# Kernel tuning notes

Hardware: AMD Instinct MI355X
Metric: run time of the kernel (lower is better)

Reference implementation:

```python
import jax, jax.numpy as jnp
import numpy as np

B, T, D, H, FF = 4, 2048, 1024, 16, 4096
HD = D // H
EPS = 1e-5


def layernorm(x, g, b):
    m = jnp.mean(x, axis=-1, keepdims=True)
    v = jnp.var(x, axis=-1, keepdims=True)
    return (x - m) * jax.lax.rsqrt(v + EPS) * g + b


def setup_inputs() -> dict:
    key = jax.random.key(0)
    ks = jax.random.split(key, 12)
    s = lambda fan_in: 1.0 / np.sqrt(fan_in)
    x = jax.random.normal(ks[0], (B, T, D), dtype=jnp.float32)
    mask = jnp.tril(jnp.ones((T, T), dtype=jnp.int32))[None, None]  # [1,1,T,T] causal
    return {
        "x": x,
        "mask": mask,
        "ln1_g": jnp.ones((D,), jnp.float32),
        "ln1_b": jnp.zeros((D,), jnp.float32),
        "ln2_g": jnp.ones((D,), jnp.float32),
        "ln2_b": jnp.zeros((D,), jnp.float32),
        "qkv_w": jax.random.normal(ks[1], (D, 3 * D), jnp.float32) * s(D),
        "out_w": jax.random.normal(ks[2], (D, D), jnp.float32) * s(D),
        "out_b": jnp.zeros((D,), jnp.float32),
        "fc1_w": jax.random.normal(ks[3], (D, FF), jnp.float32) * s(D),
        "fc1_b": jnp.zeros((FF,), jnp.float32),
        "fc2_w": jax.random.normal(ks[4], (FF, D), jnp.float32) * s(FF),
        "fc2_b": jnp.zeros((D,), jnp.float32),
    }


def reference(x, mask, ln1_g, ln1_b, ln2_g, ln2_b, qkv_w, out_w, out_b,
              fc1_w, fc1_b, fc2_w, fc2_b):
    # --- attention sublayer (pre-LN) ---
    h = layernorm(x, ln1_g, ln1_b)
    qkv = h @ qkv_w  # [B,T,3D]
    q, k, v = jnp.split(qkv, 3, axis=-1)
    q = q.reshape(B, T, H, HD).transpose(0, 2, 1, 3)  # [B,H,T,hd]
    k = k.reshape(B, T, H, HD).transpose(0, 2, 1, 3)
    v = v.reshape(B, T, H, HD).transpose(0, 2, 1, 3)
    scale = 1.0 / np.sqrt(HD)
    scores = jnp.einsum('bhqd,bhkd->bhqk', q, k) * scale  # [B,H,T,T]
    scores = jnp.where(mask == 0, -jnp.inf, scores)
    attn = jax.nn.softmax(scores, axis=-1)
    o = jnp.einsum('bhqk,bhkd->bhqd', attn, v)
    o = o.transpose(0, 2, 1, 3).reshape(B, T, D)
    x = x + (o @ out_w + out_b)
    # --- MLP sublayer (pre-LN) ---
    h = layernorm(x, ln2_g, ln2_b)
    h = jax.nn.gelu(h @ fc1_w + fc1_b, approximate=False)
    x = x + (h @ fc2_w + fc2_b)
    return x
```

## Files before the change

### kernel.cpp

```cpp
#include <hip/hip_runtime.h>

typedef unsigned short bfraw;
typedef __attribute__((ext_vector_type(8))) short short8;
typedef __attribute__((ext_vector_type(4))) float f32x4;

__device__ __forceinline__ float b2f(bfraw u){ return __uint_as_float(((unsigned int)u)<<16); }
__device__ __forceinline__ bfraw f2b(float f){
  unsigned int u = __float_as_uint(f);
  return (bfraw)((u + 0x7FFFu + ((u>>16)&1u)) >> 16);
}
__device__ __forceinline__ void store_out(float* p, float v){ *p = v; }
__device__ __forceinline__ void store_out(bfraw* p, float v){ *p = f2b(v); }
__device__ __forceinline__ void gload_lds16(const bfraw* g, short* l) {
  __builtin_amdgcn_global_load_lds((const __attribute__((address_space(1))) void*)g,
                                   (__attribute__((address_space(3))) void*)l, 16, 0, 0);
}

__global__ __launch_bounds__(1024) void transpose_f32_bf16(const float* __restrict__ in,
                                                           bfraw* __restrict__ out,
                                                           int R, int C) {
  __shared__ bfraw tile[64][65];
  const int tx = threadIdx.x, ty = threadIdx.y;
  const int c0 = blockIdx.x*64, r0 = blockIdx.y*64;
  #pragma unroll
  for (int u = 0; u < 4; ++u)
    tile[ty + u*16][tx] = f2b(in[(size_t)(r0 + ty + u*16)*C + c0 + tx]);
  __syncthreads();
  #pragma unroll
  for (int u = 0; u < 4; ++u)
    out[(size_t)(c0 + ty + u*16)*R + r0 + tx] = tile[tx][ty + u*16];
}

__global__ __launch_bounds__(256) void ln_kernel(const float* __restrict__ x,
                                                 const float* __restrict__ g,
                                                 const float* __restrict__ b,
                                                 bfraw* __restrict__ out) {
  const int row = blockIdx.x, tid = threadIdx.x;
  const f32x4 v = ((const f32x4*)(x + (size_t)row*1024))[tid];
  float s  = v[0]+v[1]+v[2]+v[3];
  float s2 = v[0]*v[0]+v[1]*v[1]+v[2]*v[2]+v[3]*v[3];
  #pragma unroll
  for (int off = 1; off < 64; off <<= 1) { s += __shfl_xor(s, off); s2 += __shfl_xor(s2, off); }
  __shared__ float red[8];
  const int wv = tid>>6, ln_ = tid&63;
  if (ln_ == 0) { red[wv] = s; red[4+wv] = s2; }
  __syncthreads();
  float a  = red[0]+red[1]+red[2]+red[3];
  float a2 = red[4]+red[5]+red[6]+red[7];
  float mean = a*(1.0f/1024.0f);
  float var  = a2*(1.0f/1024.0f) - mean*mean;
  float inv  = rsqrtf(var + 1e-5f);
  const f32x4 gr = ((const f32x4*)g)[tid];
  const f32x4 br = ((const f32x4*)b)[tid];
  ushort4 o4;
  o4.x = f2b((v[0]-mean)*inv*gr[0] + br[0]);
  o4.y = f2b((v[1]-mean)*inv*gr[1] + br[1]);
  o4.z = f2b((v[2]-mean)*inv*gr[2] + br[2]);
  o4.w = f2b((v[3]-mean)*inv*gr[3] + br[3]);
  ((ushort4*)(out + (size_t)row*1024))[tid] = o4;
}

template<int EPI, typename OutT>
__global__ __launch_bounds__(256) void gemm_bt(const bfraw* __restrict__ A,
                                               const bfraw* __restrict__ Bt,
                                               const float* __restrict__ bias,
                                               const float* __restrict__ resid,
                                               OutT* __restrict__ C,
                                               int M, int N, int K) {
  __shared__ __align__(16) short As[128*32];
  __shared__ __align__(16) short Bs[128*32];
  const int tid = threadIdx.x;
  const int wave = tid>>6, lane = tid&63;
  const int wm = wave>>1, wn = wave&1;
  const int q = lane>>4, r = lane&15;
  const int bm = blockIdx.x, bn = blockIdx.y;

  const int m0 = tid>>2, c0 = tid&3;
  const bfraw* Ag0 = A  + (size_t)(bm*128      + m0)*K + c0*8;
  const bfraw* Ag1 = A  + (size_t)(bm*128 + 64 + m0)*K + c0*8;
  const bfraw* Bg0 = Bt + (size_t)(bn*128      + m0)*K + c0*8;
  const bfraw* Bg1 = Bt + (size_t)(bn*128 + 64 + m0)*K + c0*8;
  short* Al0 = &As[tid*8];
  short* Al1 = &As[(256+tid)*8];
  short* Bl0 = &Bs[tid*8];
  short* Bl1 = &Bs[(256+tid)*8];

  f32x4 acc[4][4];
  #pragma unroll
  for (int mi = 0; mi < 4; ++mi)
    #pragma unroll
    for (int ni = 0; ni < 4; ++ni)
      acc[mi][ni] = (f32x4){0.f, 0.f, 0.f, 0.f};

  for (int k0 = 0; k0 < K; k0 += 32) {
    __syncthreads();
    gload_lds16(Ag0 + k0, Al0);
    gload_lds16(Ag1 + k0, Al1);
    gload_lds16(Bg0 + k0, Bl0);
    gload_lds16(Bg1 + k0, Bl1);
    __syncthreads();
    short8 af[4], bfr[4];
    #pragma unroll
    for (int mi = 0; mi < 4; ++mi)
      af[mi] = *(const short8*)&As[(wm*64 + mi*16 + r)*32 + q*8];
    #pragma unroll
    for (int ni = 0; ni < 4; ++ni)
      bfr[ni] = *(const short8*)&Bs[(wn*64 + ni*16 + r)*32 + q*8];
    #pragma unroll
    for (int mi = 0; mi < 4; ++mi)
      #pragma unroll
      for (int ni = 0; ni < 4; ++ni)
        acc[mi][ni] = __builtin_amdgcn_mfma_f32_16x16x32_bf16(af[mi], bfr[ni], acc[mi][ni], 0, 0, 0);
  }

  #pragma unroll
  for (int mi = 0; mi < 4; ++mi) {
    #pragma unroll
    for (int ni = 0; ni < 4; ++ni) {
      const int gcol = bn*128 + wn*64 + ni*16 + r;
      float bv = 0.f;
      if constexpr (EPI != 0) bv = bias[gcol];
      #pragma unroll
      for (int rg = 0; rg < 4; ++rg) {
        const int grow = bm*128 + wm*64 + mi*16 + q*4 + rg;
        float val = acc[mi][ni][rg];
        if constexpr (EPI != 0) val += bv;
        if constexpr (EPI == 2) val = 0.5f*val*(1.0f + erff(val*0.70710678118654752f));
        if constexpr (EPI == 1) val += resid[(size_t)grow*N + gcol];
        store_out(&C[(size_t)grow*N + gcol], val);
      }
    }
  }
}

__global__ __launch_bounds__(256) void flash_attn(const bfraw* __restrict__ qkv,
                                                  bfraw* __restrict__ o) {
  __shared__ __align__(16) short Ksh[4096];
  __shared__ __align__(16) short Vts[4096];
  __shared__ __align__(16) short Psh[4096];
  const int tid = threadIdx.x;
  const int w = tid >> 6, lane = tid & 63;
  const int r = lane & 15, qd = lane >> 4;
  const int bb = blockIdx.y >> 4, h = blockIdx.y & 15;
  const size_t hb = (size_t)bb * 2048;
  short* Pw = &Psh[w * 1024];
  const int f0 = tid, f1 = tid + 256;
  const int key0 = f0 >> 3, dc0 = (f0 & 7) * 8;
  const int key1 = f1 >> 3, dc1 = (f1 & 7) * 8;

  for (int pass = 0; pass < 2; ++pass) {
    const int qt = pass ? (31 - (int)blockIdx.x) : (int)blockIdx.x;
    const int q0 = qt * 64;
    const int ntile = qt + 1;

    short8 qf[2];
    {
      const bfraw* qrow = qkv + (hb + q0 + w*16 + r) * 3072 + h*64;
      qf[0] = *(const short8*)(qrow + qd*8);
      qf[1] = *(const short8*)(qrow + qd*8 + 32);
    }

    f32x4 oacc[4];
    #pragma unroll
    for (int nt = 0; nt < 4; ++nt) oacc[nt] = (f32x4){0.f,0.f,0.f,0.f};
    float m_i[4] = {-3.0e38f,-3.0e38f,-3.0e38f,-3.0e38f};
    float l_i[4] = {0.f,0.f,0.f,0.f};

    short8 kpre[2], vpre[2];
    {
      const bfraw* b0 = qkv + (hb + key0) * 3072 + h*64 + dc0;
      const bfraw* b1 = qkv + (hb + key1) * 3072 + h*64 + dc1;
      kpre[0] = *(const short8*)(b0 + 1024); vpre[0] = *(const short8*)(b0 + 2048);
      kpre[1] = *(const short8*)(b1 + 1024); vpre[1] = *(const short8*)(b1 + 2048);
    }

    for (int t = 0; t < ntile; ++t) {
      __syncthreads();
      #pragma unroll
      for (int pz = 0; pz < 2; ++pz) {
        const int key = pz ? key1 : key0, dc = pz ? dc1 : dc0;
        *(short8*)&Ksh[key*64 + ((((dc>>3) ^ (key>>3)) & 7) << 3)] = kpre[pz];
        const int kg = key >> 3, k7 = key & 7, dg = dc >> 3;
        #pragma unroll
        for (int i2 = 0; i2 < 8; ++i2)
          Vts[(dc + i2)*64 + (((kg ^ dg) & 7) << 3) + k7] = vpre[pz][i2];
      }
      __syncthreads();
      if (t + 1 < ntile) {
        const int j0n = (t + 1) * 64;
        const bfraw* b0 = qkv + (hb + j0n + key0) * 3072 + h*64 + dc0;
        const bfraw* b1 = qkv + (hb + j0n + key1) * 3072 + h*64 + dc1;
        kpre[0] = *(const short8*)(b0 + 1024); vpre[0] = *(const short8*)(b0 + 2048);
        kpre[1] = *(const short8*)(b1 + 1024); vpre[1] = *(const short8*)(b1 + 2048);
      }

      f32x4 s4[4];
      #pragma unroll
      for (int kt = 0; kt < 4; ++kt) {
        f32x4 a = (f32x4){0.f,0.f,0.f,0.f};
        const int key = kt*16 + r, kgk = key >> 3;
        #pragma unroll
        for (int ks = 0; ks < 2; ++ks) {
          short8 bf8 = *(const short8*)&Ksh[key*64 + ((((qd + ks*4) ^ kgk) & 7) << 3)];
          a = __builtin_amdgcn_mfma_f32_16x16x32_bf16(qf[ks], bf8, a, 0, 0, 0);
        }
        s4[kt] = a;
      }
      const bool diag = (t == qt);
      #pragma unroll
      for (int kt = 0; kt < 4; ++kt)
        #pragma unroll
        for (int rg = 0; rg < 4; ++rg) {
          float v = s4[kt][rg] * 0.125f;
          if (diag && (kt*16 + r > w*16 + qd*4 + rg)) v = -3.0e38f;
          s4[kt][rg] = v;
        }
      float alpha[4];
      #pragma unroll
      for (int rg = 0; rg < 4; ++rg) {
        float v = fmaxf(fmaxf(s4[0][rg], s4[1][rg]), fmaxf(s4[2][rg], s4[3][rg]));
        v = fmaxf(v, __shfl_xor(v, 1));
        v = fmaxf(v, __shfl_xor(v, 2));
        v = fmaxf(v, __shfl_xor(v, 4));
        v = fmaxf(v, __shfl_xor(v, 8));
        const float mn = fmaxf(m_i[rg], v);
        alpha[rg] = __expf(m_i[rg] - mn);
        m_i[rg] = mn;
        l_i[rg] *= alpha[rg];
      }
      float lsum[4] = {0.f,0.f,0.f,0.f};
      #pragma unroll
      for (int kt = 0; kt < 4; ++kt) {
        const int kg2 = kt*2 + (r >> 3), k7b = r & 7;
        #pragma unroll
        for (int rg = 0; rg < 4; ++rg) {
          const float p = __expf(s4[kt][rg] - m_i[rg]);
          lsum[rg] += p;
          const int row = qd*4 + rg;
          Pw[row*64 + (((kg2 ^ (row & 7)) & 7) << 3) + k7b] = (short)f2b(p);
        }
      }
      #pragma unroll
      for (int rg = 0; rg < 4; ++rg) {
        float v = lsum[rg];
        v += __shfl_xor(v, 1); v += __shfl_xor(v, 2);
        v += __shfl_xor(v, 4); v += __shfl_xor(v, 8);
        l_i[rg] += v;
        #pragma unroll
        for (int nt = 0; nt < 4; ++nt) oacc[nt][rg] *= alpha[rg];
      }
      short8 pf[2];
      #pragma unroll
      for (int ks = 0; ks < 2; ++ks)
        pf[ks] = *(const short8*)&Pw[r*64 + ((((qd + ks*4) ^ (r & 7)) & 7) << 3)];
      #pragma unroll
      for (int nt = 0; nt < 4; ++nt) {
        const int d = nt*16 + r, dg = d >> 3;
        #pragma unroll
        for (int ks = 0; ks < 2; ++ks) {
          short8 vf = *(const short8*)&Vts[d*64 + ((((qd + ks*4) ^ dg) & 7) << 3)];
          oacc[nt] = __builtin_amdgcn_mfma_f32_16x16x32_bf16(pf[ks], vf, oacc[nt], 0, 0, 0);
        }
      }
    }

    float invl[4];
    #pragma unroll
    for (int rg = 0; rg < 4; ++rg) invl[rg] = 1.0f / l_i[rg];
    #pragma unroll
    for (int nt = 0; nt < 4; ++nt)
      #pragma unroll
      for (int rg = 0; rg < 4; ++rg)
        o[(hb + q0 + w*16 + qd*4 + rg) * 1024 + h*64 + nt*16 + r] = f2b(oacc[nt][rg] * invl[rg]);
  }
}

extern "C" void kernel_launch(void* const* d_in, const int* in_sizes, int n_in,
                              void* d_out, int out_size, void* d_ws, size_t ws_size,
                              hipStream_t stream) {
  (void)in_sizes; (void)n_in;
  const float* x    = (const float*)d_in[0];
  const float* ln1g = (const float*)d_in[2];
  const float* ln1b = (const float*)d_in[3];
  const float* ln2g = (const float*)d_in[4];
  const float* ln2b = (const float*)d_in[5];
  const float* qkvw = (const float*)d_in[6];
  const float* outw = (const float*)d_in[7];
  const float* outb = (const float*)d_in[8];
  const float* fc1w = (const float*)d_in[9];
  const float* fc1b = (const float*)d_in[10];
  const float* fc2w = (const float*)d_in[11];
  const float* fc2b = (const float*)d_in[12];
  float* out = (float*)d_out;

  char* ws = (char*)d_ws;
  size_t off = 0;
  auto alloc = [&](size_t bytes) -> void* { void* p = ws + off; off += (bytes + 255) & ~(size_t)255; return p; };
  bfraw* wt_qkv = (bfraw*)alloc(3072ULL*1024*2);
  bfraw* wt_out = (bfraw*)alloc(1024ULL*1024*2);
  bfraw* wt_fc1 = (bfraw*)alloc(4096ULL*1024*2);
  bfraw* wt_fc2 = (bfraw*)alloc(1024ULL*4096*2);
  bfraw* hbuf   = (bfraw*)alloc(8192ULL*1024*2);
  float* x1     = (float*)alloc(8192ULL*1024*4);
  char*  big    = (char*) alloc(8192ULL*3072*2 + 8192ULL*1024*2);
  bfraw* qkv  = (bfraw*)big;
  bfraw* obuf = (bfraw*)(big + 8192ULL*3072*2);
  bfraw* hf   = (bfraw*)big;

  if (off > ws_size) {
    (void)hipMemsetAsync(d_out, 0x7F, (size_t)out_size*4, stream);
    return;
  }

  dim3 tb(64, 16);
  transpose_f32_bf16<<<dim3(48, 16), tb, 0, stream>>>(qkvw, wt_qkv, 1024, 3072);
  transpose_f32_bf16<<<dim3(16, 16), tb, 0, stream>>>(outw, wt_out, 1024, 1024);
  transpose_f32_bf16<<<dim3(64, 16), tb, 0, stream>>>(fc1w, wt_fc1, 1024, 4096);
  transpose_f32_bf16<<<dim3(16, 64), tb, 0, stream>>>(fc2w, wt_fc2, 4096, 1024);

  ln_kernel<<<8192, 256, 0, stream>>>(x, ln1g, ln1b, hbuf);
  gemm_bt<0, bfraw><<<dim3(64, 24), 256, 0, stream>>>(hbuf, wt_qkv, nullptr, nullptr, qkv, 8192, 3072, 1024);
  flash_attn<<<dim3(16, 64), 256, 0, stream>>>(qkv, obuf);
  gemm_bt<1, float><<<dim3(64, 8), 256, 0, stream>>>(obuf, wt_out, outb, x, x1, 8192, 1024, 1024);
  ln_kernel<<<8192, 256, 0, stream>>>(x1, ln2g, ln2b, hbuf);
  gemm_bt<2, bfraw><<<dim3(64, 32), 256, 0, stream>>>(hbuf, wt_fc1, fc1b, nullptr, hf, 8192, 4096, 1024);
  gemm_bt<1, float><<<dim3(64, 8), 256, 0, stream>>>(hf, wt_fc2, fc2b, x1, out, 8192, 1024, 4096);
}
```

Before: 645.9 us.

## Transpose attention MFMA operands so each lane owns one query row

Swaps the A/B operands of both MFMAs in the attention kernel so the accumulators hold S^T and O^T. Each lane then owns a single query row, which turns the per-row softmax max/sum into in-register reductions plus two cross-lane shuffles instead of four per row, and lets P and O be packed with v_cvt_pk_bf16 and stored as 8-byte vectors. It also raises wave priority around the MFMA sections with s_setprio. The causal mask index and the P LDS layout are rewritten to match, which risks indexing mistakes.

```diff
diff --git a/kernel.cpp b/kernel.cpp
--- a/kernel.cpp
+++ b/kernel.cpp
@@ -14,6 +14,11 @@
 __device__ __forceinline__ void gload_lds16(const bfraw* g, short* l) {
   __builtin_amdgcn_global_load_lds((const __attribute__((address_space(1))) void*)g,
                                    (__attribute__((address_space(3))) void*)l, 16, 0, 0);
+}
+__device__ __forceinline__ unsigned int cvt_pk_bf16(float a, float b) {
+  unsigned int r;
+  asm("v_cvt_pk_bf16_f32 %0, %1, %2" : "=v"(r) : "v"(a), "v"(b));
+  return r;
 }
 
 __global__ __launch_bounds__(1024) void transpose_f32_bf16(const float* __restrict__ in,
@@ -163,8 +168,8 @@
     f32x4 oacc[4];
     #pragma unroll
     for (int nt = 0; nt < 4; ++nt) oacc[nt] = (f32x4){0.f,0.f,0.f,0.f};
-    float m_i[4] = {-3.0e38f,-3.0e38f,-3.0e38f,-3.0e38f};
-    float l_i[4] = {0.f,0.f,0.f,0.f};
+    float m_i = -3.0e38f;
+    float l_i = 0.f;
 
     short8 kpre[2], vpre[2];
     {
@@ -195,83 +200,89 @@
       }
 
       f32x4 s4[4];
+      __builtin_amdgcn_s_setprio(1);
       #pragma unroll
       for (int kt = 0; kt < 4; ++kt) {
         f32x4 a = (f32x4){0.f,0.f,0.f,0.f};
         const int key = kt*16 + r, kgk = key >> 3;
         #pragma unroll
         for (int ks = 0; ks < 2; ++ks) {
-          short8 bf8 = *(const short8*)&Ksh[key*64 + ((((qd + ks*4) ^ kgk) & 7) << 3)];
-          a = __builtin_amdgcn_mfma_f32_16x16x32_bf16(qf[ks], bf8, a, 0, 0, 0);
+          short8 kf8 = *(const short8*)&Ksh[key*64 + ((((qd + ks*4) ^ kgk) & 7) << 3)];
+          a = __builtin_amdgcn_mfma_f32_16x16x32_bf16(kf8, qf[ks], a, 0, 0, 0);
         }
         s4[kt] = a;
       }
+      __builtin_amdgcn_s_setprio(0);
+
       const bool diag = (t == qt);
       #pragma unroll
       for (int kt = 0; kt < 4; ++kt)
         #pragma unroll
         for (int rg = 0; rg < 4; ++rg) {
           float v = s4[kt][rg] * 0.125f;
-          if (diag && (kt*16 + r > w*16 + qd*4 + rg)) v = -3.0e38f;
+          if (diag && (kt*16 + qd*4 + rg > w*16 + r)) v = -3.0e38f;
           s4[kt][rg] = v;
         }
-      float alpha[4];
-      #pragma unroll
-      for (int rg = 0; rg < 4; ++rg) {
-        float v = fmaxf(fmaxf(s4[0][rg], s4[1][rg]), fmaxf(s4[2][rg], s4[3][rg]));
-        v = fmaxf(v, __shfl_xor(v, 1));
-        v = fmaxf(v, __shfl_xor(v, 2));
-        v = fmaxf(v, __shfl_xor(v, 4));
-        v = fmaxf(v, __shfl_xor(v, 8));
-        const float mn = fmaxf(m_i[rg], v);
-        alpha[rg] = __expf(m_i[rg] - mn);
-        m_i[rg] = mn;
-        l_i[rg] *= alpha[rg];
-      }
-      float lsum[4] = {0.f,0.f,0.f,0.f};
+
+      float mx = s4[0][0];
+      #pragma unroll
+      for (int kt = 0; kt < 4; ++kt)
+        #pragma unroll
+        for (int rg = 0; rg < 4; ++rg) mx = fmaxf(mx, s4[kt][rg]);
+      mx = fmaxf(mx, __shfl_xor(mx, 16));
+      mx = fmaxf(mx, __shfl_xor(mx, 32));
+      const float mn = fmaxf(m_i, mx);
+      const float alpha = __expf(m_i - mn);
+      m_i = mn;
+      l_i *= alpha;
+
+      float lsum = 0.f;
       #pragma unroll
       for (int kt = 0; kt < 4; ++kt) {
-        const int kg2 = kt*2 + (r >> 3), k7b = r & 7;
-        #pragma unroll
-        for (int rg = 0; rg < 4; ++rg) {
-          const float p = __expf(s4[kt][rg] - m_i[rg]);
-          lsum[rg] += p;
-          const int row = qd*4 + rg;
-          Pw[row*64 + (((kg2 ^ (row & 7)) & 7) << 3) + k7b] = (short)f2b(p);
-        }
-      }
-      #pragma unroll
-      for (int rg = 0; rg < 4; ++rg) {
-        float v = lsum[rg];
-        v += __shfl_xor(v, 1); v += __shfl_xor(v, 2);
-        v += __shfl_xor(v, 4); v += __shfl_xor(v, 8);
-        l_i[rg] += v;
-        #pragma unroll
-        for (int nt = 0; nt < 4; ++nt) oacc[nt][rg] *= alpha[rg];
-      }
+        const float p0 = __expf(s4[kt][0] - mn);
+        const float p1 = __expf(s4[kt][1] - mn);
+        const float p2 = __expf(s4[kt][2] - mn);
+        const float p3 = __expf(s4[kt][3] - mn);
+        lsum += (p0 + p1) + (p2 + p3);
+        uint2 pk;
+        pk.x = cvt_pk_bf16(p0, p1);
+        pk.y = cvt_pk_bf16(p2, p3);
+        *(uint2*)((char*)Pw + r*128 + ((((kt*2 + (qd>>1)) ^ (r&7)) & 7) << 4) + ((qd&1)<<3)) = pk;
+      }
+      lsum += __shfl_xor(lsum, 16);
+      lsum += __shfl_xor(lsum, 32);
+      l_i += lsum;
+      #pragma unroll
+      for (int nt = 0; nt < 4; ++nt)
+        #pragma unroll
+        for (int rg = 0; rg < 4; ++rg) oacc[nt][rg] *= alpha;
+
       short8 pf[2];
       #pragma unroll
       for (int ks = 0; ks < 2; ++ks)
         pf[ks] = *(const short8*)&Pw[r*64 + ((((qd + ks*4) ^ (r & 7)) & 7) << 3)];
+      __builtin_amdgcn_s_setprio(1);
       #pragma unroll
       for (int nt = 0; nt < 4; ++nt) {
         const int d = nt*16 + r, dg = d >> 3;
         #pragma unroll
         for (int ks = 0; ks < 2; ++ks) {
           short8 vf = *(const short8*)&Vts[d*64 + ((((qd + ks*4) ^ dg) & 7) << 3)];
-          oacc[nt] = __builtin_amdgcn_mfma_f32_16x16x32_bf16(pf[ks], vf, oacc[nt], 0, 0, 0);
+          oacc[nt] = __builtin_amdgcn_mfma_f32_16x16x32_bf16(vf, pf[ks], oacc[nt], 0, 0, 0);
         }
       }
-    }
-
-    float invl[4];
-    #pragma unroll
-    for (int rg = 0; rg < 4; ++rg) invl[rg] = 1.0f / l_i[rg];
-    #pragma unroll
-    for (int nt = 0; nt < 4; ++nt)
-      #pragma unroll
-      for (int rg = 0; rg < 4; ++rg)
-        o[(hb + q0 + w*16 + qd*4 + rg) * 1024 + h*64 + nt*16 + r] = f2b(oacc[nt][rg] * invl[rg]);
+      __builtin_amdgcn_s_setprio(0);
+    }
+
+    const float invl = 1.0f / l_i;
+    bfraw* orow = o + (hb + q0 + w*16 + r) * 1024 + h*64;
+    #pragma unroll
+    for (int nt = 0; nt < 4; ++nt) {
+      uint2 ov;
+      ov.x = cvt_pk_bf16(oacc[nt][0]*invl, oacc[nt][1]*invl);
+      ov.y = cvt_pk_bf16(oacc[nt][2]*invl, oacc[nt][3]*invl);
+      *(uint2*)(orow + nt*16 + qd*4) = ov;
+    }
   }
 }
 
```

Result: faster. 591.4 us (-8.4%).
